# Kernel optimization log

Measured on AMD Instinct MI355X. Metric: run time of the kernel, lower is better.

Reference implementation:

```python
import jax, jax.numpy as jnp
import numpy as np

EPS = 1e-12
LN_EPS = 1e-5
RIDGE = 0.01
M, L, T = 256, 4096, 2048


def setup_inputs() -> dict:
    key = jax.random.key(0)
    ks = jax.random.split(key, 16)
    inp = {
        "gamma": jax.random.uniform(ks[0], (L,), dtype=jnp.float32),
        "A_re": jax.random.normal(ks[1], (M, L), dtype=jnp.float32),
        "A_im": jax.random.normal(ks[2], (M, L), dtype=jnp.float32),
        "X_re": jax.random.normal(ks[3], (M, T), dtype=jnp.float32),
        "X_im": jax.random.normal(ks[4], (M, T), dtype=jnp.float32),
        # LayerNorm(L) params
        "ln_w": jnp.ones((L,), jnp.float32),
        "ln_b": jnp.zeros((L,), jnp.float32),
        # MultiheadAttention(embed_dim=1, num_heads=1): in_proj [3,1]->[3], out_proj [1,1]->[1]
        "in_w": jax.random.normal(ks[5], (3,), dtype=jnp.float32),
        "in_b": jnp.zeros((3,), jnp.float32),
        "out_w": jax.random.normal(ks[6], (1,), dtype=jnp.float32),
        "out_b": jnp.zeros((1,), jnp.float32),
        # gate Linear(L, L)
        "gate_W": jax.random.normal(ks[7], (L, L), dtype=jnp.float32) * (1.0 / np.sqrt(L)),
        "gate_b": jnp.zeros((L,), jnp.float32),
        # learned scalars
        "delta": jnp.float32(0.5),
        "lmbda": jnp.float32(0.01),
    }
    return inp


def _iaa_forward(gamma, A_re, A_im, X_re, X_im, ln_w, ln_b, in_w, in_b,
                 out_w, out_b, gate_W, gate_b, delta, lmbda):
    A = (A_re + 1j * A_im).astype(jnp.complex64)      # [M, L]
    X = (X_re + 1j * X_im).astype(jnp.complex64)      # [M, T]
    p = gamma                                         # [L]

    # R = A diag(p) A^H + ridge * I   (MxM)
    AP = A * p[None, :].astype(A.dtype)
    R = AP @ A.conj().T + RIDGE * jnp.eye(M, dtype=A.dtype)
    Rinv = jnp.linalg.inv(R)                          # [M, M]

    Ah = A.conj().T                                   # [L, M]
    ARi = Ah @ Rinv                                   # [L, M]
    S = ARi @ X                                       # [L, T]
    q = jnp.sum(jnp.abs(S) ** 2, axis=1)              # [L]
    d = jnp.real(jnp.sum(ARi * Ah, axis=1))           # [L]
    v = q / (d + EPS)

    # constrain_gamma -> sigmoid(delta); use_residual
    dlt = jax.nn.sigmoid(delta)
    u = p + dlt * (v - p)

    # LayerNorm over the full length-L vector
    mu = jnp.mean(u)
    var = jnp.mean((u - mu) ** 2)
    u_p = (u - mu) / jnp.sqrt(var + LN_EPS) * ln_w + ln_b

    # MultiheadAttention(embed_dim=1, num_heads=1) over seq of L tokens, scale = 1/sqrt(1) = 1
    qv = u_p * in_w[0] + in_b[0]                      # [L]
    kv = u_p * in_w[1] + in_b[1]
    vv = u_p * in_w[2] + in_b[2]
    scores = qv[:, None] * kv[None, :]                # [L, L]
    attn = jax.nn.softmax(scores, axis=-1)
    attn_out = (attn @ vv) * out_w[0] + out_b[0]      # [L]

    # gating on u (pre-layernorm), as in the torch code
    g = jax.nn.sigmoid(gate_W @ u + gate_b)           # Linear: u @ W.T + b, u is 1-D -> W @ u + b
    r = g * v + (1.0 - g) * p

    s = r + attn_out
    return jax.nn.relu(s - lmbda)


def reference(gamma, A_re, A_im, X_re, X_im, ln_w, ln_b, in_w, in_b,
              out_w, out_b, gate_W, gate_b, delta, lmbda):
    return _iaa_forward(gamma, A_re, A_im, X_re, X_im, ln_w, ln_b, in_w, in_b,
                        out_w, out_b, gate_W, gate_b, delta, lmbda)
```

## Files before the change

### kernel.cpp

```cpp
#include <hip/hip_runtime.h>
#include <hip/hip_bf16.h>
#include <math.h>

#define MM 256
#define LL 4096
#define TT 2048

typedef __attribute__((ext_vector_type(8))) short bf16x8;
typedef __attribute__((ext_vector_type(4))) float f32x4;
typedef __attribute__((ext_vector_type(4))) unsigned short us4;
typedef unsigned short ushort_t;

#define OFF_Q      262144
#define OFF_D      266240
#define OFF_V      270336
#define OFF_U      274432
#define OFF_UP     278528
#define OFF_RINVP  290816
#define OFF_GP     421888
#define OFF_APL    552960
#define OFF_XPL    2650112
#define OFF_ATP    3698688
#define OFF_WTP    5795840
#define OFF_PA     5795840
#define OFF_PX     8417280
#define OFF_XA     9990144
#define OFF_XB     10121216
#define OFF_EA     10252288
#define OFF_EB     10383360

#define MFMA3(ACC, AH, AL, BH, BL)                                              \
  ACC = __builtin_amdgcn_mfma_f32_16x16x32_bf16(AH, BH, ACC, 0, 0, 0);          \
  ACC = __builtin_amdgcn_mfma_f32_16x16x32_bf16(AH, BL, ACC, 0, 0, 0);          \
  ACC = __builtin_amdgcn_mfma_f32_16x16x32_bf16(AL, BH, ACC, 0, 0, 0);

__device__ __forceinline__ void split_bf16(float x, ushort_t& h, ushort_t& l) {
  __hip_bfloat16 bh = __float2bfloat16(x);
  h = *(ushort_t*)&bh;
  __hip_bfloat16 bl = __float2bfloat16(x - __bfloat162float(bh));
  l = *(ushort_t*)&bl;
}
__device__ __forceinline__ float bfu2f(ushort_t u) {
  unsigned v = ((unsigned)u) << 16;
  float f;
  __builtin_memcpy(&f, &v, 4);
  return f;
}

__device__ __forceinline__ void tile_ij(int t, int& ti, int& tj) {
  float f = sqrtf(8.0f * (float)t + 1.0f);
  ti = (int)((f - 1.0f) * 0.5f + 0.001f);
  tj = t - ((ti * (ti + 1)) >> 1);
}

__device__ __forceinline__ float wave_red_sum(float v) {
#pragma unroll
  for (int o = 32; o > 0; o >>= 1) v += __shfl_down(v, o);
  return v;
}
__device__ __forceinline__ float wave_red_max(float v) {
#pragma unroll
  for (int o = 32; o > 0; o >>= 1) v = fmaxf(v, __shfl_down(v, o));
  return v;
}
__device__ float blk_red_sum(float v) {
  __shared__ float sh[4];
  int lane = threadIdx.x & 63, wv = threadIdx.x >> 6;
  v = wave_red_sum(v);
  __syncthreads();
  if (lane == 0) sh[wv] = v;
  __syncthreads();
  return sh[0] + sh[1] + sh[2] + sh[3];
}
__device__ float blk_red_max(float v) {
  __shared__ float shm[4];
  int lane = threadIdx.x & 63, wv = threadIdx.x >> 6;
  v = wave_red_max(v);
  __syncthreads();
  if (lane == 0) shm[wv] = v;
  __syncthreads();
  return fmaxf(fmaxf(shm[0], shm[1]), fmaxf(shm[2], shm[3]));
}

__device__ __forceinline__ float2 r_mirror(const float2* __restrict__ R, int i, int j) {
  if ((i >> 6) >= (j >> 6)) return R[i * 256 + j];
  float2 r = R[j * 256 + i];
  r.y = -r.y;
  return r;
}

__global__ __launch_bounds__(256) void k_prep(float* __restrict__ ws,
                                              const float* __restrict__ Are,
                                              const float* __restrict__ Aim,
                                              const float* __restrict__ Xre,
                                              const float* __restrict__ Xim,
                                              const float* __restrict__ gamma) {
  __shared__ float tr[32][33], ti[32][33];
  int bid = blockIdx.x, tid = threadIdx.x;
  if (bid < 8) {
    ((float4*)(ws + OFF_Q))[bid * 256 + tid] = make_float4(0.f, 0.f, 0.f, 0.f);
  } else if (bid < 1032) {
    int i4 = (bid - 8) * 256 + tid;
    ushort_t* dst = (ushort_t*)(ws + OFF_APL);
    float4 re = ((const float4*)Are)[i4];
    float4 im = ((const float4*)Aim)[i4];
    float4 ga = ((const float4*)gamma)[i4 & (LL / 4 - 1)];
    float sr[4] = {re.x * sqrtf(ga.x), re.y * sqrtf(ga.y), re.z * sqrtf(ga.z), re.w * sqrtf(ga.w)};
    float si[4] = {im.x * sqrtf(ga.x), im.y * sqrtf(ga.y), im.z * sqrtf(ga.z), im.w * sqrtf(ga.w)};
    us4 hr, lr, hi, li;
#pragma unroll
    for (int e = 0; e < 4; ++e) {
      ushort_t h, l;
      split_bf16(sr[e], h, l); hr[e] = h; lr[e] = l;
      split_bf16(si[e], h, l); hi[e] = h; li[e] = l;
    }
    size_t o = (size_t)i4 * 4;
    *(us4*)(dst + o) = hr;
    *(us4*)(dst + (size_t)MM * LL + o) = lr;
    *(us4*)(dst + 2 * (size_t)MM * LL + o) = hi;
    *(us4*)(dst + 3 * (size_t)MM * LL + o) = li;
  } else if (bid < 1544) {
    int i4 = (bid - 1032) * 256 + tid;
    ushort_t* dst = (ushort_t*)(ws + OFF_XPL);
    float4 re = ((const float4*)Xre)[i4];
    float4 im = ((const float4*)Xim)[i4];
    float fr[4] = {re.x, re.y, re.z, re.w};
    float fi[4] = {im.x, im.y, im.z, im.w};
    us4 hr, lr, hi, li;
#pragma unroll
    for (int e = 0; e < 4; ++e) {
      ushort_t h, l;
      split_bf16(fr[e], h, l); hr[e] = h; lr[e] = l;
      split_bf16(fi[e], h, l); hi[e] = h; li[e] = l;
    }
    size_t o = (size_t)i4 * 4;
    *(us4*)(dst + o) = hr;
    *(us4*)(dst + (size_t)MM * TT + o) = lr;
    *(us4*)(dst + 2 * (size_t)MM * TT + o) = hi;
    *(us4*)(dst + 3 * (size_t)MM * TT + o) = li;
  } else {
    int b2 = bid - 1544;
    ushort_t* dst = (ushort_t*)(ws + OFF_ATP);
    int c0 = (b2 & 127) * 32, r0 = (b2 >> 7) * 32;
    int tx = tid & 31, tg = tid >> 5;
#pragma unroll
    for (int i = 0; i < 4; ++i) {
      int r = tg + 8 * i;
      tr[r][tx] = Are[(size_t)(r0 + r) * LL + c0 + tx];
      ti[r][tx] = Aim[(size_t)(r0 + r) * LL + c0 + tx];
    }
    __syncthreads();
#pragma unroll
    for (int i = 0; i < 4; ++i) {
      int rr = tg + 8 * i;
      size_t o = (size_t)(c0 + rr) * 256 + r0 + tx;
      ushort_t h, l;
      split_bf16(tr[tx][rr], h, l);
      dst[o] = h;
      dst[o + 1048576] = l;
      split_bf16(ti[tx][rr], h, l);
      dst[o + 2097152] = h;
      dst[o + 3145728] = l;
    }
  }
}

__global__ __launch_bounds__(256, 4) void k_gram_both(float* __restrict__ ws) {
  __shared__ __align__(16) ushort_t sA[4][64][40];
  __shared__ __align__(16) ushort_t sB[4][64][40];
  const int ti_lu[10] = {0, 1, 1, 2, 2, 2, 3, 3, 3, 3};
  const int tj_lu[10] = {0, 0, 1, 0, 1, 2, 0, 1, 2, 3};
  int bid = blockIdx.x;
  const ushort_t* pl;
  float2* P;
  int K, tile, ksplit;
  size_t PS;
  if (bid < 320) {
    pl = (const ushort_t*)(ws + OFF_APL);
    P = (float2*)(ws + OFF_PA) + (size_t)bid * 4096;
    K = LL;
    PS = (size_t)MM * LL;
    tile = bid % 10;
    ksplit = bid / 10;
  } else {
    int b2 = bid - 320;
    pl = (const ushort_t*)(ws + OFF_XPL);
    P = (float2*)(ws + OFF_PX) + (size_t)b2 * 4096;
    K = TT;
    PS = (size_t)MM * TT;
    tile = b2 % 10;
    ksplit = b2 / 10;
  }
  int kbeg = ksplit * 128;
  int i0 = ti_lu[tile] * 64, j0 = tj_lu[tile] * 64;
  bool diag = (i0 == j0);
  int tid = threadIdx.x;
  int lane = tid & 63, wv = tid >> 6;
  int srow = tid >> 2, sslot = tid & 3;
  int arow = wv * 16 + (lane & 15);
  int kq = (lane >> 4) * 8;
  f32x4 z = {0.f, 0.f, 0.f, 0.f};
  f32x4 Zrr[4], Zri[4], Zir[4], Zii[4];
#pragma unroll
  for (int s = 0; s < 4; ++s) { Zrr[s] = z; Zri[s] = z; Zir[s] = z; Zii[s] = z; }

  for (int chunk = 0; chunk < 4; ++chunk) {
    int k0 = kbeg + chunk * 32;
    __syncthreads();
#pragma unroll
    for (int p = 0; p < 4; ++p) {
      *(bf16x8*)&sA[p][srow][sslot * 8] =
          *(const bf16x8*)(pl + p * PS + (size_t)(i0 + srow) * K + k0 + sslot * 8);
      if (!diag)
        *(bf16x8*)&sB[p][srow][sslot * 8] =
            *(const bf16x8*)(pl + p * PS + (size_t)(j0 + srow) * K + k0 + sslot * 8);
    }
    __syncthreads();
    bf16x8 arh = *(const bf16x8*)&sA[0][arow][kq];
    bf16x8 arl = *(const bf16x8*)&sA[1][arow][kq];
    bf16x8 aih = *(const bf16x8*)&sA[2][arow][kq];
    bf16x8 ail = *(const bf16x8*)&sA[3][arow][kq];
    ushort_t(*bs)[64][40] = diag ? sA : sB;
#pragma unroll
    for (int s = 0; s < 4; ++s) {
      int brow = s * 16 + (lane & 15);
      bf16x8 brh = *(const bf16x8*)&bs[0][brow][kq];
      bf16x8 brl = *(const bf16x8*)&bs[1][brow][kq];
      bf16x8 bih = *(const bf16x8*)&bs[2][brow][kq];
      bf16x8 bil = *(const bf16x8*)&bs[3][brow][kq];
      MFMA3(Zrr[s], arh, arl, brh, brl);
      MFMA3(Zri[s], arh, arl, bih, bil);
      MFMA3(Zir[s], aih, ail, brh, brl);
      MFMA3(Zii[s], aih, ail, bih, bil);
    }
  }
  int lrb = wv * 16 + (lane >> 4) * 4;
#pragma unroll
  for (int s = 0; s < 4; ++s) {
    int lc = s * 16 + (lane & 15);
#pragma unroll
    for (int r = 0; r < 4; ++r) {
      float re = Zrr[s][r] + Zii[s][r];
      float im = Zir[s][r] - Zri[s][r];
      P[(lrb + r) * 64 + lc] = make_float2(re, im);
    }
  }
}

__global__ __launch_bounds__(256) void k_reduce(float* __restrict__ ws) {
  int bid = blockIdx.x, tid = threadIdx.x;
  if (bid < 160) {
    const float2* PA = (const float2*)(ws + OFF_PA);
    float2* R2 = (float2*)ws;
    int t = bid >> 4;
    int e = ((bid & 15) << 8) + tid;
    float sx = 0.f, sy = 0.f;
#pragma unroll 4
    for (int k = 0; k < 32; ++k) {
      float2 p = PA[(size_t)(k * 10 + t) * 4096 + e];
      sx += p.x; sy += p.y;
    }
    int ti, tj;
    tile_ij(t, ti, tj);
    int i = ti * 64 + (e >> 6), j = tj * 64 + (e & 63);
    if (i == j) sx += 0.01f;
    R2[i * 256 + j] = make_float2(sx, sy);
  } else {
    const float2* PX = (const float2*)(ws + OFF_PX);
    ushort_t* dst = (ushort_t*)(ws + OFF_GP);
    int idx = (bid - 160) * 256 + tid;
    int i = idx >> 8, j = idx & 255;
    int ii = i, jj = j;
    float sgn = 1.f;
    if ((i >> 6) < (j >> 6)) { ii = j; jj = i; sgn = -1.f; }
    int ti = ii >> 6, tj = jj >> 6;
    int t = ((ti * (ti + 1)) >> 1) + tj;
    int e = ((ii & 63) << 6) + (jj & 63);
    float sx = 0.f, sy = 0.f;
#pragma unroll 4
    for (int k = 0; k < 16; ++k) {
      float2 p = PX[(size_t)(k * 10 + t) * 4096 + e];
      sx += p.x; sy += p.y;
    }
    sy *= sgn;
    ushort_t h, l;
    split_bf16(sx, h, l);
    dst[idx] = h;
    dst[idx + 65536] = l;
    split_bf16(sy, h, l);
    dst[idx + 131072] = h;
    dst[idx + 196608] = l;
  }
}

__global__ __launch_bounds__(256) void k_n1(float* __restrict__ ws) {
  __shared__ float2 As[16][17], Bs[16][17];
  const float2* R = (const float2*)ws;
  int bid = blockIdx.x, tid = threadIdx.x;
  if (bid < 256) {
    float2* E1 = (float2*)(ws + OFF_EA);
    int i0 = (bid >> 4) * 16, j0 = (bid & 15) * 16;
    int tx = tid & 15, ty = tid >> 4;
    int rowA = i0 + ty;
    float DiA = R[rowA * 257].x;
    float accx = 0.f, accy = 0.f;
    for (int k0 = 0; k0 < 256; k0 += 16) {
      __syncthreads();
      {
        int c = k0 + tx;
        float2 r = r_mirror(R, rowA, c);
        float dl = (rowA == c) ? 1.0f : 0.0f;
        As[ty][tx] = make_float2(dl - r.x / DiA, -r.y / DiA);
      }
      {
        int rB = k0 + ty, c = j0 + tx;
        float DiB = R[rB * 257].x;
        float2 r = r_mirror(R, rB, c);
        float dl = (rB == c) ? 1.0f : 0.0f;
        Bs[ty][tx] = make_float2(dl - r.x / DiB, -r.y / DiB);
      }
      __syncthreads();
#pragma unroll
      for (int kk = 0; kk < 16; ++kk) {
        float2 a = As[ty][kk], bb = Bs[kk][tx];
        accx += a.x * bb.x - a.y * bb.y;
        accy += a.x * bb.y + a.y * bb.x;
      }
    }
    E1[rowA * 256 + j0 + tx] = make_float2(accx, accy);
  } else {
    float2* X1 = (float2*)(ws + OFF_XA);
    int idx = (bid - 256) * 256 + tid;
    int i = idx >> 8, j = idx & 255;
    float Dii = R[i * 257].x;
    float Djj = R[j * 257].x;
    float2 r = r_mirror(R, i, j);
    float dl = (i == j) ? 1.0f : 0.0f;
    float ex = dl - r.x / Dii;
    float ey = -r.y / Dii;
    X1[idx] = make_float2((dl + ex) / Djj, ey / Djj);
  }
}

__global__ __launch_bounds__(256) void k_newt_step(const float2* __restrict__ Xin,
                                                   const float2* __restrict__ Ein,
                                                   float2* __restrict__ Xout,
                                                   float2* __restrict__ Eout, int xblocks) {
  __shared__ float2 As[16][17], Bs[16][17];
  int bid = blockIdx.x;
  bool isX = bid < xblocks;
  int b = isX ? bid : bid - xblocks;
  const float2* Bm = isX ? Xin : Ein;
  int i0 = (b >> 4) * 16, j0 = (b & 15) * 16;
  int tx = threadIdx.x & 15, ty = threadIdx.x >> 4;
  float accx = 0.f, accy = 0.f;
  for (int k0 = 0; k0 < 256; k0 += 16) {
    __syncthreads();
    As[ty][tx] = Ein[(i0 + ty) * 256 + k0 + tx];
    Bs[ty][tx] = Bm[(k0 + ty) * 256 + j0 + tx];
    __syncthreads();
#pragma unroll
    for (int kk = 0; kk < 16; ++kk) {
      float2 a = As[ty][kk], bb = Bs[kk][tx];
      accx += a.x * bb.x - a.y * bb.y;
      accy += a.x * bb.y + a.y * bb.x;
    }
  }
  int idx = (i0 + ty) * 256 + j0 + tx;
  if (isX) {
    float2 x = Xin[idx];
    Xout[idx] = make_float2(x.x + accx, x.y + accy);
  } else {
    Eout[idx] = make_float2(accx, accy);
  }
}

__global__ __launch_bounds__(256) void k_newt_fin(const float2* __restrict__ Xin,
                                                  const float2* __restrict__ Ein,
                                                  ushort_t* __restrict__ dst) {
  __shared__ float2 As[16][17], Bs[16][17];
  int b = blockIdx.x;
  int i0 = (b >> 4) * 16, j0 = (b & 15) * 16;
  int tx = threadIdx.x & 15, ty = threadIdx.x >> 4;
  float accx = 0.f, accy = 0.f;
  for (int k0 = 0; k0 < 256; k0 += 16) {
    __syncthreads();
    As[ty][tx] = Ein[(i0 + ty) * 256 + k0 + tx];
    Bs[ty][tx] = Xin[(k0 + ty) * 256 + j0 + tx];
    __syncthreads();
#pragma unroll
    for (int kk = 0; kk < 16; ++kk) {
      float2 a = As[ty][kk], bb = Bs[kk][tx];
      accx += a.x * bb.x - a.y * bb.y;
      accy += a.x * bb.y + a.y * bb.x;
    }
  }
  int idx = (i0 + ty) * 256 + j0 + tx;
  float2 x = Xin[idx];
  float vx = x.x + accx, vy = x.y + accy;
  ushort_t h, l;
  split_bf16(vx, h, l);
  dst[idx] = h;
  dst[idx + 65536] = l;
  split_bf16(vy, h, l);
  dst[idx + 131072] = h;
  dst[idx + 196608] = l;
}

__global__ __launch_bounds__(256) void k_wide_mfma(const ushort_t* __restrict__ Ap,
                                                   const ushort_t* __restrict__ Bp,
                                                   const float* __restrict__ AuxRe,
                                                   const float* __restrict__ AuxIm,
                                                   ushort_t* __restrict__ WTout,
                                                   float* __restrict__ dq, int mode) {
  __shared__ __align__(16) ushort_t sB[4][32][40];
  const ushort_t* arh_p = Ap;
  const ushort_t* arl_p = Ap + 65536;
  const ushort_t* aih_p = Ap + 131072;
  const ushort_t* ail_p = Ap + 196608;
  const ushort_t* brh_p = Bp;
  const ushort_t* brl_p = Bp + 1048576;
  const ushort_t* bih_p = Bp + 2097152;
  const ushort_t* bil_p = Bp + 3145728;
  int j0 = blockIdx.x * 32;
  int i0 = blockIdx.y * 64;
  int tid = threadIdx.x;
  int lane = tid & 63, wv = tid >> 6;
  int spos = tid & 127;
  int srow = spos >> 2, sslot = spos & 3;
  int p0 = (tid >> 7) * 2;
  const ushort_t* bp0 = (p0 == 0) ? brh_p : bih_p;
  const ushort_t* bp1 = (p0 == 0) ? brl_p : bil_p;
  int m = i0 + wv * 16 + (lane & 15);
  int kq = (lane >> 4) * 8;
  f32x4 z = {0.f, 0.f, 0.f, 0.f};
  f32x4 Zrr[2], Zri[2], Zir[2], Zii[2];
#pragma unroll
  for (int s = 0; s < 2; ++s) { Zrr[s] = z; Zri[s] = z; Zir[s] = z; Zii[s] = z; }
  for (int k0 = 0; k0 < 256; k0 += 32) {
    __syncthreads();
    {
      size_t bo = (size_t)(j0 + srow) * 256 + k0 + sslot * 8;
      *(bf16x8*)&sB[p0][srow][sslot * 8] = *(const bf16x8*)(bp0 + bo);
      *(bf16x8*)&sB[p0 + 1][srow][sslot * 8] = *(const bf16x8*)(bp1 + bo);
    }
    __syncthreads();
    size_t ao = (size_t)m * 256 + k0 + kq;
    bf16x8 arh = *(const bf16x8*)(arh_p + ao);
    bf16x8 arl = *(const bf16x8*)(arl_p + ao);
    bf16x8 aih = *(const bf16x8*)(aih_p + ao);
    bf16x8 ail = *(const bf16x8*)(ail_p + ao);
#pragma unroll
    for (int s = 0; s < 2; ++s) {
      int brow = s * 16 + (lane & 15);
      bf16x8 brh = *(const bf16x8*)&sB[0][brow][kq];
      bf16x8 brl = *(const bf16x8*)&sB[1][brow][kq];
      bf16x8 bih = *(const bf16x8*)&sB[2][brow][kq];
      bf16x8 bil = *(const bf16x8*)&sB[3][brow][kq];
      MFMA3(Zrr[s], arh, arl, brh, brl);
      MFMA3(Zri[s], arh, arl, bih, bil);
      MFMA3(Zir[s], aih, ail, brh, brl);
      MFMA3(Zii[s], aih, ail, bih, bil);
    }
  }
  int rbase = i0 + wv * 16 + (lane >> 4) * 4;
#pragma unroll
  for (int s = 0; s < 2; ++s) {
    int col = j0 + s * 16 + (lane & 15);
    size_t wo = (size_t)col * 256 + rbase;
    float part = 0.f;
    if (mode == 0) {
      us4 hr, lr, hi, li;
#pragma unroll
      for (int r = 0; r < 4; ++r) {
        float re = Zrr[s][r] - Zii[s][r];
        float im = Zri[s][r] + Zir[s][r];
        ushort_t h, l;
        split_bf16(re, h, l);
        hr[r] = h; lr[r] = l;
        split_bf16(im, h, l);
        hi[r] = h; li[r] = l;
        size_t o = (size_t)(rbase + r) * LL + col;
        part += re * AuxRe[o] - im * AuxIm[o];
      }
      *(us4*)(WTout + wo) = hr;
      *(us4*)(WTout + 1048576 + wo) = lr;
      *(us4*)(WTout + 2097152 + wo) = hi;
      *(us4*)(WTout + 3145728 + wo) = li;
    } else {
      us4 wh = *(const us4*)(brh_p + wo);
      us4 wl = *(const us4*)(brl_p + wo);
      us4 wih = *(const us4*)(bih_p + wo);
      us4 wil = *(const us4*)(bil_p + wo);
#pragma unroll
      for (int r = 0; r < 4; ++r) {
        float re = Zrr[s][r] - Zii[s][r];
        float im = Zri[s][r] + Zir[s][r];
        float wx = bfu2f(wh[r]) + bfu2f(wl[r]);
        float wy = bfu2f(wih[r]) + bfu2f(wil[r]);
        part += wx * re + wy * im;
      }
    }
    part += __shfl_down(part, 32);
    part += __shfl_down(part, 16);
    if ((lane >> 4) == 0) atomicAdd(dq + col, part);
  }
}

__global__ __launch_bounds__(256) void k_uvln(float* __restrict__ ws,
                                              const float* __restrict__ gamma,
                                              const float* __restrict__ delta,
                                              const float* __restrict__ lnw,
                                              const float* __restrict__ lnb) {
  const float* q = ws + OFF_Q;
  const float* d = ws + OFF_D;
  float* vvec = ws + OFF_V;
  float* uvec = ws + OFF_U;
  float* up = ws + OFF_UP;
  int tid = threadIdx.x;
  float dlt = 1.0f / (1.0f + expf(-delta[0]));
  float s = 0.f;
  for (int i = tid; i < LL; i += 256) {
    float v = q[i] / (d[i] + 1e-12f);
    float p = gamma[i];
    float u = p + dlt * (v - p);
    vvec[i] = v;
    uvec[i] = u;
    s += u;
  }
  float mu = blk_red_sum(s) * (1.0f / LL);
  float s2 = 0.f;
  for (int i = tid; i < LL; i += 256) { float dd = uvec[i] - mu; s2 += dd * dd; }
  float var = blk_red_sum(s2) * (1.0f / LL);
  float inv = rsqrtf(var + 1e-5f);
  for (int i = tid; i < LL; i += 256) up[i] = (uvec[i] - mu) * inv * lnw[i] + lnb[i];
}

__global__ __launch_bounds__(256) void k_gateattn(const float* __restrict__ ws,
                                                  const float* __restrict__ Wg,
                                                  const float* __restrict__ gb,
                                                  const float* __restrict__ inw,
                                                  const float* __restrict__ inb,
                                                  const float* __restrict__ outw,
                                                  const float* __restrict__ outb,
                                                  const float* __restrict__ gamma,
                                                  const float* __restrict__ lmbda,
                                                  float* __restrict__ out) {
  const float* uvec = ws + OFF_U;
  const float* up = ws + OFF_UP;
  const float* vvec = ws + OFF_V;
  int i = blockIdx.x, tid = threadIdx.x;
  const float4* wr = (const float4*)(Wg + (size_t)i * LL);
  const float4* u4 = (const float4*)uvec;
  float s = 0.f;
  for (int j = tid; j < LL / 4; j += 256) {
    float4 w = wr[j], x = u4[j];
    s += w.x * x.x + w.y * x.y + w.z * x.z + w.w * x.w;
  }
  float tot = blk_red_sum(s);
  float g = 1.0f / (1.0f + expf(-(tot + gb[i])));
  float qv = up[i] * inw[0] + inb[0];
  float w1 = inw[1], b1 = inb[1], w2 = inw[2], b2 = inb[2];
  const float4* up4 = (const float4*)up;
  float mx = -3.4e38f;
  for (int j = tid; j < LL / 4; j += 256) {
    float4 u = up4[j];
    mx = fmaxf(mx, fmaxf(fmaxf(qv * (u.x * w1 + b1), qv * (u.y * w1 + b1)),
                         fmaxf(qv * (u.z * w1 + b1), qv * (u.w * w1 + b1))));
  }
  mx = blk_red_max(mx);
  float den = 0.f, num = 0.f;
  for (int j = tid; j < LL / 4; j += 256) {
    float4 u = up4[j];
    float e0 = expf(qv * (u.x * w1 + b1) - mx);
    float e1 = expf(qv * (u.y * w1 + b1) - mx);
    float e2 = expf(qv * (u.z * w1 + b1) - mx);
    float e3 = expf(qv * (u.w * w1 + b1) - mx);
    den += e0 + e1 + e2 + e3;
    num += e0 * (u.x * w2 + b2) + e1 * (u.y * w2 + b2) + e2 * (u.z * w2 + b2) + e3 * (u.w * w2 + b2);
  }
  den = blk_red_sum(den);
  num = blk_red_sum(num);
  if (tid == 0) {
    float attn = (num / den) * outw[0] + outb[0];
    float r = g * vvec[i] + (1.0f - g) * gamma[i] + attn - lmbda[0];
    out[i] = fmaxf(r, 0.0f);
  }
}

extern "C" void kernel_launch(void* const* d_in, const int* in_sizes, int n_in,
                              void* d_out, int out_size, void* d_ws, size_t ws_size,
                              hipStream_t stream) {
  const float* gamma = (const float*)d_in[0];
  const float* Are   = (const float*)d_in[1];
  const float* Aim   = (const float*)d_in[2];
  const float* Xre   = (const float*)d_in[3];
  const float* Xim   = (const float*)d_in[4];
  const float* lnw   = (const float*)d_in[5];
  const float* lnb   = (const float*)d_in[6];
  const float* inw   = (const float*)d_in[7];
  const float* inb   = (const float*)d_in[8];
  const float* outw  = (const float*)d_in[9];
  const float* outb  = (const float*)d_in[10];
  const float* gateW = (const float*)d_in[11];
  const float* gateb = (const float*)d_in[12];
  const float* delta = (const float*)d_in[13];
  const float* lmbda = (const float*)d_in[14];
  float* out = (float*)d_out;
  float* ws = (float*)d_ws;

  float2* XA = (float2*)(ws + OFF_XA);
  float2* XB = (float2*)(ws + OFF_XB);
  float2* EA = (float2*)(ws + OFF_EA);
  float2* EB = (float2*)(ws + OFF_EB);
  ushort_t* Rinvp = (ushort_t*)(ws + OFF_RINVP);

  k_prep<<<2568, 256, 0, stream>>>(ws, Are, Aim, Xre, Xim, gamma);
  k_gram_both<<<480, 256, 0, stream>>>(ws);
  k_reduce<<<416, 256, 0, stream>>>(ws);
  k_n1<<<512, 256, 0, stream>>>(ws);
  k_newt_step<<<512, 256, 0, stream>>>(XA, EA, XB, EB, 256);
  k_newt_step<<<512, 256, 0, stream>>>(XB, EB, XA, EA, 256);
  k_newt_step<<<512, 256, 0, stream>>>(XA, EA, XB, EB, 256);
  k_newt_fin<<<256, 256, 0, stream>>>(XB, EB, Rinvp);

  k_wide_mfma<<<dim3(128, 4), 256, 0, stream>>>(Rinvp, (ushort_t*)(ws + OFF_ATP),
                                                Are, Aim, (ushort_t*)(ws + OFF_WTP),
                                                ws + OFF_D, 0);
  k_wide_mfma<<<dim3(128, 4), 256, 0, stream>>>((ushort_t*)(ws + OFF_GP),
                                                (ushort_t*)(ws + OFF_WTP),
                                                nullptr, nullptr, nullptr, ws + OFF_Q, 1);
  k_uvln<<<1, 256, 0, stream>>>(ws, gamma, delta, lnw, lnb);
  k_gateattn<<<LL, 256, 0, stream>>>(ws, gateW, gateb, inw, inb, outw, outb, gamma, lmbda, out);
}
```

Baseline: 293.8 us.

## Move Newton-Schulz inverse iterations to split-bf16 MFMA with transposed operand layouts

The Newton iteration for the 256x256 complex inverse moves off scalar FP32 LDS-tiled matmuls onto MFMA bf16x3 split-precision kernels. Operands are stored as hi/lo bf16 planes in both row-major and transposed layouts, so each step writes the formats the next step needs. The first E^2 product becomes its own step, and the layernorm kernel now runs with 1024 threads and vectorised float4 loads. The change cuts scalar FLOP cost in the serial inverse chain, but uses fewer blocks per launch (32-64) and risks precision loss from bf16 splitting in the iteration.

```diff
diff --git a/kernel.cpp b/kernel.cpp
--- a/kernel.cpp
+++ b/kernel.cpp
@@ -24,10 +24,11 @@
 #define OFF_WTP    5795840
 #define OFF_PA     5795840
 #define OFF_PX     8417280
-#define OFF_XA     9990144
-#define OFF_XB     10121216
-#define OFF_EA     10252288
-#define OFF_EB     10383360
+#define OFF_E0P    9990144
+#define OFF_EAP    10252288
+#define OFF_EBP    10514432
+#define OFF_XAT    10776576
+#define OFF_XBT    10907648
 
 #define MFMA3(ACC, AH, AL, BH, BL)                                              \
   ACC = __builtin_amdgcn_mfma_f32_16x16x32_bf16(AH, BH, ACC, 0, 0, 0);          \
@@ -293,118 +294,131 @@
   }
 }
 
-__global__ __launch_bounds__(256) void k_n1(float* __restrict__ ws) {
-  __shared__ float2 As[16][17], Bs[16][17];
+__global__ __launch_bounds__(256) void k_n1p(float* __restrict__ ws) {
   const float2* R = (const float2*)ws;
-  int bid = blockIdx.x, tid = threadIdx.x;
-  if (bid < 256) {
-    float2* E1 = (float2*)(ws + OFF_EA);
-    int i0 = (bid >> 4) * 16, j0 = (bid & 15) * 16;
-    int tx = tid & 15, ty = tid >> 4;
-    int rowA = i0 + ty;
-    float DiA = R[rowA * 257].x;
-    float accx = 0.f, accy = 0.f;
-    for (int k0 = 0; k0 < 256; k0 += 16) {
-      __syncthreads();
-      {
-        int c = k0 + tx;
-        float2 r = r_mirror(R, rowA, c);
-        float dl = (rowA == c) ? 1.0f : 0.0f;
-        As[ty][tx] = make_float2(dl - r.x / DiA, -r.y / DiA);
+  ushort_t* e0 = (ushort_t*)(ws + OFF_E0P);
+  ushort_t* e0t = e0 + 262144;
+  ushort_t* x1t = (ushort_t*)(ws + OFF_XAT);
+  int idx = blockIdx.x * 256 + threadIdx.x;
+  int i = idx >> 8, j = idx & 255;
+  float Dii = R[i * 257].x, Djj = R[j * 257].x;
+  float2 r = r_mirror(R, i, j);
+  float dl = (i == j) ? 1.0f : 0.0f;
+  float ex = dl - r.x / Dii, ey = -r.y / Dii;
+  float xx = (dl + ex) / Djj, xy = ey / Djj;
+  int rm = i * 256 + j, trn = j * 256 + i;
+  ushort_t h, l;
+  split_bf16(ex, h, l);
+  e0[rm] = h; e0[rm + 65536] = l;
+  e0t[trn] = h; e0t[trn + 65536] = l;
+  split_bf16(ey, h, l);
+  e0[rm + 131072] = h; e0[rm + 196608] = l;
+  e0t[trn + 131072] = h; e0t[trn + 196608] = l;
+  split_bf16(xx, h, l);
+  x1t[trn] = h; x1t[trn + 65536] = l;
+  split_bf16(xy, h, l);
+  x1t[trn + 131072] = h; x1t[trn + 196608] = l;
+}
+
+__global__ __launch_bounds__(256) void k_prim(const ushort_t* __restrict__ Arm,
+                                              const ushort_t* __restrict__ BtrE,
+                                              const ushort_t* __restrict__ BtrX,
+                                              const ushort_t* __restrict__ AddX,
+                                              ushort_t* __restrict__ EoutRm,
+                                              ushort_t* __restrict__ EoutTr,
+                                              ushort_t* __restrict__ XoutTr,
+                                              ushort_t* __restrict__ XoutRm,
+                                              int nEjobs) {
+  __shared__ __align__(16) ushort_t sB[4][32][40];
+  int job = blockIdx.x;
+  bool isE = job < nEjobs;
+  int b = isE ? job : job - nEjobs;
+  const ushort_t* Bp = isE ? BtrE : BtrX;
+  const ushort_t* Add = isE ? (const ushort_t*)nullptr : AddX;
+  ushort_t* Otr = isE ? EoutTr : XoutTr;
+  ushort_t* Orm = isE ? EoutRm : XoutRm;
+  int j0 = (b & 7) * 32, i0 = (b >> 3) * 64;
+  int tid = threadIdx.x;
+  int lane = tid & 63, wv = tid >> 6;
+  int spos = tid & 127;
+  int srow = spos >> 2, sslot = spos & 3;
+  int p0 = (tid >> 7) * 2;
+  int m = i0 + wv * 16 + (lane & 15);
+  int kq = (lane >> 4) * 8;
+  f32x4 z = {0.f, 0.f, 0.f, 0.f};
+  f32x4 Zrr[2], Zri[2], Zir[2], Zii[2];
+#pragma unroll
+  for (int s = 0; s < 2; ++s) { Zrr[s] = z; Zri[s] = z; Zir[s] = z; Zii[s] = z; }
+  for (int k0 = 0; k0 < 256; k0 += 32) {
+    __syncthreads();
+    {
+      size_t bo = (size_t)(j0 + srow) * 256 + k0 + sslot * 8;
+      *(bf16x8*)&sB[p0][srow][sslot * 8] =
+          *(const bf16x8*)(Bp + (size_t)p0 * 65536 + bo);
+      *(bf16x8*)&sB[p0 + 1][srow][sslot * 8] =
+          *(const bf16x8*)(Bp + (size_t)(p0 + 1) * 65536 + bo);
+    }
+    __syncthreads();
+    size_t ao = (size_t)m * 256 + k0 + kq;
+    bf16x8 arh = *(const bf16x8*)(Arm + ao);
+    bf16x8 arl = *(const bf16x8*)(Arm + 65536 + ao);
+    bf16x8 aih = *(const bf16x8*)(Arm + 131072 + ao);
+    bf16x8 ail = *(const bf16x8*)(Arm + 196608 + ao);
+#pragma unroll
+    for (int s = 0; s < 2; ++s) {
+      int brow = s * 16 + (lane & 15);
+      bf16x8 brh = *(const bf16x8*)&sB[0][brow][kq];
+      bf16x8 brl = *(const bf16x8*)&sB[1][brow][kq];
+      bf16x8 bih = *(const bf16x8*)&sB[2][brow][kq];
+      bf16x8 bil = *(const bf16x8*)&sB[3][brow][kq];
+      MFMA3(Zrr[s], arh, arl, brh, brl);
+      MFMA3(Zri[s], arh, arl, bih, bil);
+      MFMA3(Zir[s], aih, ail, brh, brl);
+      MFMA3(Zii[s], aih, ail, bih, bil);
+    }
+  }
+  int rbase = i0 + wv * 16 + (lane >> 4) * 4;
+#pragma unroll
+  for (int s = 0; s < 2; ++s) {
+    int col = j0 + s * 16 + (lane & 15);
+    size_t wo = (size_t)col * 256 + rbase;
+    us4 adr, adl, adi, adj;
+    if (Add) {
+      adr = *(const us4*)(Add + wo);
+      adl = *(const us4*)(Add + 65536 + wo);
+      adi = *(const us4*)(Add + 131072 + wo);
+      adj = *(const us4*)(Add + 196608 + wo);
+    }
+    us4 hr, lr, hi, li;
+#pragma unroll
+    for (int r = 0; r < 4; ++r) {
+      float re = Zrr[s][r] - Zii[s][r];
+      float im = Zri[s][r] + Zir[s][r];
+      if (Add) {
+        re += bfu2f(adr[r]) + bfu2f(adl[r]);
+        im += bfu2f(adi[r]) + bfu2f(adj[r]);
       }
-      {
-        int rB = k0 + ty, c = j0 + tx;
-        float DiB = R[rB * 257].x;
-        float2 r = r_mirror(R, rB, c);
-        float dl = (rB == c) ? 1.0f : 0.0f;
-        Bs[ty][tx] = make_float2(dl - r.x / DiB, -r.y / DiB);
+      ushort_t h, l;
+      split_bf16(re, h, l); hr[r] = h; lr[r] = l;
+      split_bf16(im, h, l); hi[r] = h; li[r] = l;
+    }
+    if (Otr) {
+      *(us4*)(Otr + wo) = hr;
+      *(us4*)(Otr + 65536 + wo) = lr;
+      *(us4*)(Otr + 131072 + wo) = hi;
+      *(us4*)(Otr + 196608 + wo) = li;
+    }
+    if (Orm) {
+#pragma unroll
+      for (int r = 0; r < 4; ++r) {
+        size_t o = (size_t)(rbase + r) * 256 + col;
+        Orm[o] = hr[r];
+        Orm[o + 65536] = lr[r];
+        Orm[o + 131072] = hi[r];
+        Orm[o + 196608] = li[r];
       }
-      __syncthreads();
-#pragma unroll
-      for (int kk = 0; kk < 16; ++kk) {
-        float2 a = As[ty][kk], bb = Bs[kk][tx];
-        accx += a.x * bb.x - a.y * bb.y;
-        accy += a.x * bb.y + a.y * bb.x;
-      }
-    }
-    E1[rowA * 256 + j0 + tx] = make_float2(accx, accy);
-  } else {
-    float2* X1 = (float2*)(ws + OFF_XA);
-    int idx = (bid - 256) * 256 + tid;
-    int i = idx >> 8, j = idx & 255;
-    float Dii = R[i * 257].x;
-    float Djj = R[j * 257].x;
-    float2 r = r_mirror(R, i, j);
-    float dl = (i == j) ? 1.0f : 0.0f;
-    float ex = dl - r.x / Dii;
-    float ey = -r.y / Dii;
-    X1[idx] = make_float2((dl + ex) / Djj, ey / Djj);
-  }
-}
-
-__global__ __launch_bounds__(256) void k_newt_step(const float2* __restrict__ Xin,
-                                                   const float2* __restrict__ Ein,
-                                                   float2* __restrict__ Xout,
-                                                   float2* __restrict__ Eout, int xblocks) {
-  __shared__ float2 As[16][17], Bs[16][17];
-  int bid = blockIdx.x;
-  bool isX = bid < xblocks;
-  int b = isX ? bid : bid - xblocks;
-  const float2* Bm = isX ? Xin : Ein;
-  int i0 = (b >> 4) * 16, j0 = (b & 15) * 16;
-  int tx = threadIdx.x & 15, ty = threadIdx.x >> 4;
-  float accx = 0.f, accy = 0.f;
-  for (int k0 = 0; k0 < 256; k0 += 16) {
-    __syncthreads();
-    As[ty][tx] = Ein[(i0 + ty) * 256 + k0 + tx];
-    Bs[ty][tx] = Bm[(k0 + ty) * 256 + j0 + tx];
-    __syncthreads();
-#pragma unroll
-    for (int kk = 0; kk < 16; ++kk) {
-      float2 a = As[ty][kk], bb = Bs[kk][tx];
-      accx += a.x * bb.x - a.y * bb.y;
-      accy += a.x * bb.y + a.y * bb.x;
-    }
-  }
-  int idx = (i0 + ty) * 256 + j0 + tx;
-  if (isX) {
-    float2 x = Xin[idx];
-    Xout[idx] = make_float2(x.x + accx, x.y + accy);
-  } else {
-    Eout[idx] = make_float2(accx, accy);
-  }
-}
-
-__global__ __launch_bounds__(256) void k_newt_fin(const float2* __restrict__ Xin,
-                                                  const float2* __restrict__ Ein,
-                                                  ushort_t* __restrict__ dst) {
-  __shared__ float2 As[16][17], Bs[16][17];
-  int b = blockIdx.x;
-  int i0 = (b >> 4) * 16, j0 = (b & 15) * 16;
-  int tx = threadIdx.x & 15, ty = threadIdx.x >> 4;
-  float accx = 0.f, accy = 0.f;
-  for (int k0 = 0; k0 < 256; k0 += 16) {
-    __syncthreads();
-    As[ty][tx] = Ein[(i0 + ty) * 256 + k0 + tx];
-    Bs[ty][tx] = Xin[(k0 + ty) * 256 + j0 + tx];
-    __syncthreads();
-#pragma unroll
-    for (int kk = 0; kk < 16; ++kk) {
-      float2 a = As[ty][kk], bb = Bs[kk][tx];
-      accx += a.x * bb.x - a.y * bb.y;
-      accy += a.x * bb.y + a.y * bb.x;
-    }
-  }
-  int idx = (i0 + ty) * 256 + j0 + tx;
-  float2 x = Xin[idx];
-  float vx = x.x + accx, vy = x.y + accy;
-  ushort_t h, l;
-  split_bf16(vx, h, l);
-  dst[idx] = h;
-  dst[idx + 65536] = l;
-  split_bf16(vy, h, l);
-  dst[idx + 131072] = h;
-  dst[idx + 196608] = l;
+    }
+  }
 }
 
 __global__ __launch_bounds__(256) void k_wide_mfma(const ushort_t* __restrict__ Ap,
@@ -422,8 +436,9 @@
   const ushort_t* brl_p = Bp + 1048576;
   const ushort_t* bih_p = Bp + 2097152;
   const ushort_t* bil_p = Bp + 3145728;
-  int j0 = blockIdx.x * 32;
-  int i0 = blockIdx.y * 64;
+  int job = blockIdx.x;
+  int j0 = (job & 127) * 32;
+  int i0 = (job >> 7) * 64;
   int tid = threadIdx.x;
   int lane = tid & 63, wv = tid >> 6;
   int spos = tid & 127;
@@ -507,33 +522,45 @@
   }
 }
 
-__global__ __launch_bounds__(256) void k_uvln(float* __restrict__ ws,
-                                              const float* __restrict__ gamma,
-                                              const float* __restrict__ delta,
-                                              const float* __restrict__ lnw,
-                                              const float* __restrict__ lnb) {
-  const float* q = ws + OFF_Q;
-  const float* d = ws + OFF_D;
-  float* vvec = ws + OFF_V;
-  float* uvec = ws + OFF_U;
-  float* up = ws + OFF_UP;
-  int tid = threadIdx.x;
+__global__ __launch_bounds__(1024) void k_uvln(float* __restrict__ ws,
+                                               const float* __restrict__ gamma,
+                                               const float* __restrict__ delta,
+                                               const float* __restrict__ lnw,
+                                               const float* __restrict__ lnb) {
+  __shared__ float sh[16];
+  int tid = threadIdx.x, lane = tid & 63, wv = tid >> 6;
+  float4 q4 = ((const float4*)(ws + OFF_Q))[tid];
+  float4 d4 = ((const float4*)(ws + OFF_D))[tid];
+  float4 g4 = ((const float4*)gamma)[tid];
   float dlt = 1.0f / (1.0f + expf(-delta[0]));
-  float s = 0.f;
-  for (int i = tid; i < LL; i += 256) {
-    float v = q[i] / (d[i] + 1e-12f);
-    float p = gamma[i];
-    float u = p + dlt * (v - p);
-    vvec[i] = v;
-    uvec[i] = u;
-    s += u;
-  }
-  float mu = blk_red_sum(s) * (1.0f / LL);
-  float s2 = 0.f;
-  for (int i = tid; i < LL; i += 256) { float dd = uvec[i] - mu; s2 += dd * dd; }
-  float var = blk_red_sum(s2) * (1.0f / LL);
+  float v0 = q4.x / (d4.x + 1e-12f), v1 = q4.y / (d4.y + 1e-12f);
+  float v2 = q4.z / (d4.z + 1e-12f), v3 = q4.w / (d4.w + 1e-12f);
+  float u0 = g4.x + dlt * (v0 - g4.x), u1 = g4.y + dlt * (v1 - g4.y);
+  float u2 = g4.z + dlt * (v2 - g4.z), u3 = g4.w + dlt * (v3 - g4.w);
+  ((float4*)(ws + OFF_V))[tid] = make_float4(v0, v1, v2, v3);
+  ((float4*)(ws + OFF_U))[tid] = make_float4(u0, u1, u2, u3);
+  float s = wave_red_sum(u0 + u1 + u2 + u3);
+  if (lane == 0) sh[wv] = s;
+  __syncthreads();
+  float mu = 0.f;
+#pragma unroll
+  for (int w = 0; w < 16; ++w) mu += sh[w];
+  mu *= (1.0f / LL);
+  __syncthreads();
+  float d0 = u0 - mu, d1 = u1 - mu, d2 = u2 - mu, d3 = u3 - mu;
+  float s2 = wave_red_sum(d0 * d0 + d1 * d1 + d2 * d2 + d3 * d3);
+  if (lane == 0) sh[wv] = s2;
+  __syncthreads();
+  float var = 0.f;
+#pragma unroll
+  for (int w = 0; w < 16; ++w) var += sh[w];
+  var *= (1.0f / LL);
   float inv = rsqrtf(var + 1e-5f);
-  for (int i = tid; i < LL; i += 256) up[i] = (uvec[i] - mu) * inv * lnw[i] + lnb[i];
+  float4 w4 = ((const float4*)lnw)[tid];
+  float4 b4 = ((const float4*)lnb)[tid];
+  ((float4*)(ws + OFF_UP))[tid] =
+      make_float4(d0 * inv * w4.x + b4.x, d1 * inv * w4.y + b4.y,
+                  d2 * inv * w4.z + b4.z, d3 * inv * w4.w + b4.w);
 }
 
 __global__ __launch_bounds__(256) void k_gateattn(const float* __restrict__ ws,
@@ -609,27 +636,37 @@
   float* out = (float*)d_out;
   float* ws = (float*)d_ws;
 
-  float2* XA = (float2*)(ws + OFF_XA);
-  float2* XB = (float2*)(ws + OFF_XB);
-  float2* EA = (float2*)(ws + OFF_EA);
-  float2* EB = (float2*)(ws + OFF_EB);
+  ushort_t* e0rm = (ushort_t*)(ws + OFF_E0P);
+  ushort_t* e0tr = e0rm + 262144;
+  ushort_t* eArm = (ushort_t*)(ws + OFF_EAP);
+  ushort_t* eAtr = eArm + 262144;
+  ushort_t* eBrm = (ushort_t*)(ws + OFF_EBP);
+  ushort_t* eBtr = eBrm + 262144;
+  ushort_t* xAt = (ushort_t*)(ws + OFF_XAT);
+  ushort_t* xBt = (ushort_t*)(ws + OFF_XBT);
   ushort_t* Rinvp = (ushort_t*)(ws + OFF_RINVP);
 
   k_prep<<<2568, 256, 0, stream>>>(ws, Are, Aim, Xre, Xim, gamma);
   k_gram_both<<<480, 256, 0, stream>>>(ws);
   k_reduce<<<416, 256, 0, stream>>>(ws);
-  k_n1<<<512, 256, 0, stream>>>(ws);
-  k_newt_step<<<512, 256, 0, stream>>>(XA, EA, XB, EB, 256);
-  k_newt_step<<<512, 256, 0, stream>>>(XB, EB, XA, EA, 256);
-  k_newt_step<<<512, 256, 0, stream>>>(XA, EA, XB, EB, 256);
-  k_newt_fin<<<256, 256, 0, stream>>>(XB, EB, Rinvp);
-
-  k_wide_mfma<<<dim3(128, 4), 256, 0, stream>>>(Rinvp, (ushort_t*)(ws + OFF_ATP),
-                                                Are, Aim, (ushort_t*)(ws + OFF_WTP),
-                                                ws + OFF_D, 0);
-  k_wide_mfma<<<dim3(128, 4), 256, 0, stream>>>((ushort_t*)(ws + OFF_GP),
-                                                (ushort_t*)(ws + OFF_WTP),
-                                                nullptr, nullptr, nullptr, ws + OFF_Q, 1);
-  k_uvln<<<1, 256, 0, stream>>>(ws, gamma, delta, lnw, lnb);
-  k_gateattn<<<LL, 256, 0, stream>>>(ws, gateW, gateb, inw, inb, outw, outb, gamma, lmbda, out);
-}
+  k_n1p<<<256, 256, 0, stream>>>(ws);
+  k_prim<<<32, 256, 0, stream>>>(e0rm, e0tr, nullptr, nullptr,
+                                 eArm, eAtr, nullptr, nullptr, 32);
+  k_prim<<<64, 256, 0, stream>>>(eArm, eAtr, xAt, xAt,
+                                 eBrm, eBtr, xBt, nullptr, 32);
+  k_prim<<<64, 256, 0, stream>>>(eBrm, eBtr, xBt, xBt,
+                                 eArm, eAtr, xAt, nullptr, 32);
+  k_prim<<<64, 256, 0, stream>>>(eArm, eAtr, xAt, xAt,
+                                 eBrm, eBtr, xBt, nullptr, 32);
+  k_prim<<<32, 256, 0, stream>>>(eBrm, nullptr, xBt, xBt,
+                                 nullptr, nullptr, nullptr, Rinvp, 0);
+  k_wide_mfma<<<512, 256, 0, stream>>>(Rinvp, (const ushort_t*)(ws + OFF_ATP),
+                                       Are, Aim, (ushort_t*)(ws + OFF_WTP),
+                                       ws + OFF_D, 0);
+  k_wide_mfma<<<512, 256, 0, stream>>>((const ushort_t*)(ws + OFF_GP),
+                                       (const ushort_t*)(ws + OFF_WTP),
+                                       nullptr, nullptr, nullptr, ws + OFF_Q, 1);
+  k_uvln<<<1, 1024, 0, stream>>>(ws, gamma, delta, lnw, lnb);
+  k_gateattn<<<LL, 256, 0, stream>>>(ws, gateW, gateb, inw, inb, outw, outb,
+                                     gamma, lmbda, out);
+}
```

After: 256.7 us. -12.6%, faster.
